# Kernel tuning notes

Hardware: AMD Instinct MI355X
Metric: run time of the kernel (lower is better)

Reference implementation:

```python
import jax, jax.numpy as jnp
import numpy as np

DIM_V = 1024
NUM_HEADS = 64            # per the module arg name; actually the per-chunk size
DIM_SPLIT = DIM_V // NUM_HEADS  # 16 = effective number of attention heads (module quirk)
N_Q, N_K = 2048, 2048
DIM_Q, DIM_K = 1024, 1024


def setup_inputs() -> dict:
    key = jax.random.key(0)
    ks = jax.random.split(key, 10)
    s = 0.02
    return {
        "Q": jax.random.normal(ks[0], (N_Q, DIM_Q), dtype=jnp.float32),
        "K": jax.random.normal(ks[1], (N_K, DIM_K), dtype=jnp.float32),
        "Wq": jax.random.normal(ks[2], (DIM_V, DIM_Q), dtype=jnp.float32) * s,
        "bq": jax.random.normal(ks[3], (DIM_V,), dtype=jnp.float32) * s,
        "Wk": jax.random.normal(ks[4], (DIM_V, DIM_K), dtype=jnp.float32) * s,
        "bk": jax.random.normal(ks[5], (DIM_V,), dtype=jnp.float32) * s,
        "Wv": jax.random.normal(ks[6], (DIM_V, DIM_K), dtype=jnp.float32) * s,
        "bv": jax.random.normal(ks[7], (DIM_V,), dtype=jnp.float32) * s,
        "Wo": jax.random.normal(ks[8], (DIM_V, DIM_V), dtype=jnp.float32) * s,
        "bo": jax.random.normal(ks[9], (DIM_V,), dtype=jnp.float32) * s,
    }


def _split_heads(x):
    # jnp.split(x[None], DIM_SPLIT, axis=2) then concat on axis 0 ==
    # [DIM_SPLIT, n, NUM_HEADS] with chunk h = x[:, h*NUM_HEADS:(h+1)*NUM_HEADS]
    n = x.shape[0]
    return x.reshape(n, DIM_SPLIT, NUM_HEADS).transpose(1, 0, 2)


def reference(Q, K, Wq, bq, Wk, bk, Wv, bv, Wo, bo):
    q = Q @ Wq.T + bq            # [n_q, dim_V]
    k = K @ Wk.T + bk            # [n_k, dim_V]
    v = K @ Wv.T + bv            # [n_k, dim_V]
    Q_ = _split_heads(q)         # [H, n_q, d] with H=DIM_SPLIT, d=NUM_HEADS
    K_ = _split_heads(k)
    V_ = _split_heads(v)
    # Faithful to source: softmax first, THEN divide by sqrt(dim_V)
    A = jax.nn.softmax(jnp.einsum('hqd,hkd->hqk', Q_, K_), axis=-1)
    A = A / jnp.sqrt(jnp.float32(DIM_V))
    O = (Q_ + jnp.einsum('hqk,hkd->hqd', A, V_)).reshape(-1, DIM_V)  # [n_q, dim_V]
    # res1 = identity (ln=False)
    O = O + jax.nn.relu(O @ Wo.T + bo)
    # res2 = identity (ln=False)
    return O
```

## Files before the change

### kernel.cpp

```cpp
#include <hip/hip_runtime.h>
#include <hip/hip_bf16.h>
#include <cstdint>

typedef unsigned short u16;
typedef __attribute__((ext_vector_type(8))) short short8;
typedef __attribute__((ext_vector_type(4))) float f32x4;

__device__ __forceinline__ u16 f2b(float f) {
  uint32_t u = __float_as_uint(f);
  u += 0x7fffu + ((u >> 16) & 1u);
  return (u16)(u >> 16);
}
__device__ __forceinline__ float b2f(u16 b) {
  return __uint_as_float(((uint32_t)b) << 16);
}
__device__ __forceinline__ uint32_t pk2bf(float a, float b) {
  __hip_bfloat162 t = __float22bfloat162_rn(make_float2(a, b));
  return *(uint32_t*)&t;
}

__global__ __launch_bounds__(256) void cast_all(
    const float* __restrict__ Q, const float* __restrict__ K,
    const float* __restrict__ Wq, const float* __restrict__ Wk,
    const float* __restrict__ Wv, const float* __restrict__ Wo,
    u16* __restrict__ xq, u16* __restrict__ xk,
    u16* __restrict__ wq, u16* __restrict__ wk,
    u16* __restrict__ wv, u16* __restrict__ wo) {
  int g = blockIdx.x * 256 + threadIdx.x;
  const float* src; u16* dst; int off;
  if      (g <  524288) { src = Q;  dst = xq; off = g; }
  else if (g < 1048576) { src = K;  dst = xk; off = g -  524288; }
  else if (g < 1310720) { src = Wq; dst = wq; off = g - 1048576; }
  else if (g < 1572864) { src = Wk; dst = wk; off = g - 1310720; }
  else if (g < 1835008) { src = Wv; dst = wv; off = g - 1572864; }
  else                  { src = Wo; dst = wo; off = g - 1835008; }
  float4 v = reinterpret_cast<const float4*>(src)[off];
  ushort4 o4;
  o4.x = f2b(v.x); o4.y = f2b(v.y); o4.z = f2b(v.z); o4.w = f2b(v.w);
  reinterpret_cast<ushort4*>(dst)[off] = o4;
}

__global__ __launch_bounds__(256) void gemm3(
    const u16* __restrict__ xq, const u16* __restrict__ xk,
    const u16* __restrict__ wq, const u16* __restrict__ wk,
    const u16* __restrict__ wv,
    const float* __restrict__ bq, const float* __restrict__ bk,
    const float* __restrict__ bv,
    u16* __restrict__ qb, u16* __restrict__ kb, u16* __restrict__ vT) {
  __shared__ __align__(16) u16 sA[128 * 40];
  __shared__ __align__(16) u16 sB[64 * 40];
  const int t = threadIdx.x, blk = blockIdx.x, z = blockIdx.y;
  const u16 *A, *B; const float* bias; u16* C; int ldC, mbase, nbase; bool brow;
  if (z == 0)      { A = xq; B = wq; bias = bq; C = qb; ldC = 1024;
                     mbase = (blk >> 4) * 128; nbase = (blk & 15) * 64; brow = false; }
  else if (z == 1) { A = xk; B = wk; bias = bk; C = kb; ldC = 1024;
                     mbase = (blk >> 4) * 128; nbase = (blk & 15) * 64; brow = false; }
  else             { A = wv; B = xk; bias = bv; C = vT; ldC = 2048;
                     mbase = (blk >> 5) * 128; nbase = (blk & 31) * 64; brow = true; }
  const int lane = t & 63, wid = t >> 6;
  const int wy = wid >> 1, wx = wid & 1;
  const int m = lane & 15, quad = lane >> 4;

  const int arow = t >> 1, acb = (t & 1) * 16;
  const int brow_ = t >> 2, bcb = (t & 3) * 8;
  const u16* gA = A + (mbase + arow) * 1024 + acb;
  const u16* gB = B + (nbase + brow_) * 1024 + bcb;

  uint4 ra0 = *(const uint4*)(gA);
  uint4 ra1 = *(const uint4*)(gA + 8);
  uint4 rb0 = *(const uint4*)(gB);

  f32x4 acc[4][2];
#pragma unroll
  for (int i = 0; i < 4; i++)
#pragma unroll
    for (int j = 0; j < 2; j++) acc[i][j] = (f32x4){0.f, 0.f, 0.f, 0.f};

  for (int kb_ = 0; kb_ < 32; ++kb_) {
    __syncthreads();
    *(uint4*)(&sA[arow * 40 + acb])     = ra0;
    *(uint4*)(&sA[arow * 40 + acb + 8]) = ra1;
    *(uint4*)(&sB[brow_ * 40 + bcb])    = rb0;
    if (kb_ < 31) {
      ra0 = *(const uint4*)(gA + (kb_ + 1) * 32);
      ra1 = *(const uint4*)(gA + (kb_ + 1) * 32 + 8);
      rb0 = *(const uint4*)(gB + (kb_ + 1) * 32);
    }
    __syncthreads();
    short8 af[4], bf[2];
#pragma unroll
    for (int mi = 0; mi < 4; mi++)
      af[mi] = *(const short8*)(&sA[(wy * 64 + mi * 16 + m) * 40 + quad * 8]);
#pragma unroll
    for (int ni = 0; ni < 2; ni++)
      bf[ni] = *(const short8*)(&sB[(wx * 32 + ni * 16 + m) * 40 + quad * 8]);
#pragma unroll
    for (int mi = 0; mi < 4; mi++)
#pragma unroll
      for (int ni = 0; ni < 2; ni++)
        acc[mi][ni] = __builtin_amdgcn_mfma_f32_16x16x32_bf16(
            af[mi], bf[ni], acc[mi][ni], 0, 0, 0);
  }

#pragma unroll
  for (int mi = 0; mi < 4; mi++)
#pragma unroll
    for (int ni = 0; ni < 2; ni++) {
      const int col = nbase + wx * 32 + ni * 16 + m;
      const float bcol = brow ? 0.f : bias[col];
#pragma unroll
      for (int r = 0; r < 4; r++) {
        const int row = mbase + wy * 64 + mi * 16 + quad * 4 + r;
        const float bval = brow ? bias[row] : bcol;
        C[row * ldC + col] = f2b(acc[mi][ni][r] + bval);
      }
    }
}

__global__ __launch_bounds__(256) void gemm_out(
    const u16* __restrict__ A, const u16* __restrict__ B,
    const float* __restrict__ bias, const u16* __restrict__ Res,
    float* __restrict__ out) {
  __shared__ __align__(16) u16 sA[64 * 40];
  __shared__ __align__(16) u16 sB[64 * 40];
  const int t = threadIdx.x, blk = blockIdx.x;
  const int mbase = (blk >> 4) * 64, nbase = (blk & 15) * 64;
  const int lane = t & 63, wid = t >> 6;
  const int wy = wid >> 1, wx = wid & 1;
  const int m = lane & 15, quad = lane >> 4;
  const int srow = t >> 2, scb = (t & 3) * 8;
  const u16* gA = A + (mbase + srow) * 1024 + scb;
  const u16* gB = B + (nbase + srow) * 1024 + scb;
  uint4 ra = *(const uint4*)gA;
  uint4 rb = *(const uint4*)gB;

  f32x4 acc[2][2];
#pragma unroll
  for (int i = 0; i < 2; i++)
#pragma unroll
    for (int j = 0; j < 2; j++) acc[i][j] = (f32x4){0.f, 0.f, 0.f, 0.f};

  for (int kb_ = 0; kb_ < 32; ++kb_) {
    __syncthreads();
    *(uint4*)(&sA[srow * 40 + scb]) = ra;
    *(uint4*)(&sB[srow * 40 + scb]) = rb;
    if (kb_ < 31) {
      ra = *(const uint4*)(gA + (kb_ + 1) * 32);
      rb = *(const uint4*)(gB + (kb_ + 1) * 32);
    }
    __syncthreads();
    short8 af[2], bf[2];
#pragma unroll
    for (int mi = 0; mi < 2; mi++)
      af[mi] = *(const short8*)(&sA[(wy * 32 + mi * 16 + m) * 40 + quad * 8]);
#pragma unroll
    for (int ni = 0; ni < 2; ni++)
      bf[ni] = *(const short8*)(&sB[(wx * 32 + ni * 16 + m) * 40 + quad * 8]);
#pragma unroll
    for (int mi = 0; mi < 2; mi++)
#pragma unroll
      for (int ni = 0; ni < 2; ni++)
        acc[mi][ni] = __builtin_amdgcn_mfma_f32_16x16x32_bf16(
            af[mi], bf[ni], acc[mi][ni], 0, 0, 0);
  }

#pragma unroll
  for (int mi = 0; mi < 2; mi++)
#pragma unroll
    for (int ni = 0; ni < 2; ni++) {
      const int col = nbase + wx * 32 + ni * 16 + m;
      const float bcol = bias[col];
#pragma unroll
      for (int r = 0; r < 4; r++) {
        const int row = mbase + wy * 32 + mi * 16 + quad * 4 + r;
        out[row * 1024 + col] =
            b2f(Res[row * 1024 + col]) + fmaxf(acc[mi][ni][r] + bcol, 0.f);
      }
    }
}

__global__ __launch_bounds__(256) void flash(
    const u16* __restrict__ q, const u16* __restrict__ k,
    const u16* __restrict__ vT, u16* __restrict__ po, float* __restrict__ lp) {
  __shared__ __align__(16) u16 sK[64 * 72];
  __shared__ __align__(16) u16 sV[64 * 72];
  __shared__ __align__(16) u16 sP[4 * 32 * 72];
  const int t = threadIdx.x;
  const int qt = blockIdx.x, h = blockIdx.y, sp = blockIdx.z;
  const int lane = t & 63, wid = t >> 6;
  const int m = lane & 15, quad = lane >> 4;
  const int colbase = h * 64;
  const int pbase = wid * 2304;
  const int kbase = sp * 512;

  short8 aq[2][2];
#pragma unroll
  for (int mi = 0; mi < 2; mi++)
#pragma unroll
    for (int g = 0; g < 2; g++)
      aq[mi][g] = *(const short8*)(
          &q[(qt * 128 + wid * 32 + mi * 16 + m) * 1024 + colbase + g * 32 + quad * 8]);

  f32x4 o[2][4];
  float lpart[2] = {0.f, 0.f};
#pragma unroll
  for (int mi = 0; mi < 2; mi++)
#pragma unroll
    for (int nt = 0; nt < 4; nt++) o[mi][nt] = (f32x4){0.f, 0.f, 0.f, 0.f};

  const int srow = t >> 2, scb = (t & 3) * 16;
  const u16* gK = k + (kbase + srow) * 1024 + colbase + scb;
  const u16* gV = vT + (colbase + srow) * 2048 + kbase + scb;

  uint4 rk0 = *(const uint4*)(gK), rk1 = *(const uint4*)(gK + 8);
  uint4 rv0 = *(const uint4*)(gV), rv1 = *(const uint4*)(gV + 8);

  uint32_t* sP32 = (uint32_t*)sP;

  for (int kt = 0; kt < 8; ++kt) {
    __syncthreads();
    *(uint4*)(&sK[srow * 72 + scb])     = rk0;
    *(uint4*)(&sK[srow * 72 + scb + 8]) = rk1;
    *(uint4*)(&sV[srow * 72 + scb])     = rv0;
    *(uint4*)(&sV[srow * 72 + scb + 8]) = rv1;
    if (kt < 7) {
      rk0 = *(const uint4*)(gK + (kt + 1) * 65536);
      rk1 = *(const uint4*)(gK + (kt + 1) * 65536 + 8);
      rv0 = *(const uint4*)(gV + (kt + 1) * 64);
      rv1 = *(const uint4*)(gV + (kt + 1) * 64 + 8);
    }
    __syncthreads();

#pragma unroll
    for (int nt = 0; nt < 4; nt++) {
      short8 bk0 = *(const short8*)(&sK[(nt * 16 + m) * 72 + quad * 8]);
      short8 bk1 = *(const short8*)(&sK[(nt * 16 + m) * 72 + 32 + quad * 8]);
#pragma unroll
      for (int mi = 0; mi < 2; mi++) {
        f32x4 st = (f32x4){0.f, 0.f, 0.f, 0.f};
        st = __builtin_amdgcn_mfma_f32_16x16x32_bf16(bk0, aq[mi][0], st, 0, 0, 0);
        st = __builtin_amdgcn_mfma_f32_16x16x32_bf16(bk1, aq[mi][1], st, 0, 0, 0);
        float p0 = __expf(st[0] - 16.0f);
        float p1 = __expf(st[1] - 16.0f);
        float p2 = __expf(st[2] - 16.0f);
        float p3 = __expf(st[3] - 16.0f);
        lpart[mi] += (p0 + p1) + (p2 + p3);
        const int pa_ = pbase + (mi * 16 + m) * 72 + nt * 16 + quad * 4;
        sP32[pa_ >> 1]       = pk2bf(p0, p1);
        sP32[(pa_ >> 1) + 1] = pk2bf(p2, p3);
      }
    }

    short8 pa[2][2];
#pragma unroll
    for (int mi = 0; mi < 2; mi++)
#pragma unroll
      for (int g = 0; g < 2; g++)
        pa[mi][g] = *(const short8*)(&sP[pbase + (mi * 16 + m) * 72 + g * 32 + quad * 8]);
#pragma unroll
    for (int nt = 0; nt < 4; nt++) {
      short8 bv0 = *(const short8*)(&sV[(nt * 16 + m) * 72 + quad * 8]);
      short8 bv1 = *(const short8*)(&sV[(nt * 16 + m) * 72 + 32 + quad * 8]);
#pragma unroll
      for (int mi = 0; mi < 2; mi++) {
        o[mi][nt] = __builtin_amdgcn_mfma_f32_16x16x32_bf16(pa[mi][0], bv0, o[mi][nt], 0, 0, 0);
        o[mi][nt] = __builtin_amdgcn_mfma_f32_16x16x32_bf16(pa[mi][1], bv1, o[mi][nt], 0, 0, 0);
      }
    }
  }

#pragma unroll
  for (int mi = 0; mi < 2; mi++) {
    float l = lpart[mi];
    l += __shfl_xor(l, 16);
    l += __shfl_xor(l, 32);
    if (quad == 0)
      lp[(sp * 16 + h) * 2048 + qt * 128 + wid * 32 + mi * 16 + m] = l;
  }

#pragma unroll
  for (int mi = 0; mi < 2; mi++)
#pragma unroll
    for (int r = 0; r < 4; r++) {
      const int qg = qt * 128 + wid * 32 + mi * 16 + quad * 4 + r;
      const int base = ((sp * 16 + h) * 2048 + qg) * 64;
#pragma unroll
      for (int nt = 0; nt < 4; nt++)
        po[base + nt * 16 + m] = f2b(o[mi][nt][r]);
    }
}

__global__ __launch_bounds__(256) void combine(
    const u16* __restrict__ po, const float* __restrict__ lp,
    const u16* __restrict__ qb, u16* __restrict__ ob) {
  const int idx = blockIdx.x * 256 + threadIdx.x;
  const int dq = idx & 15, qg = (idx >> 4) & 2047, h = idx >> 15;
  float acc0 = 0.f, acc1 = 0.f, acc2 = 0.f, acc3 = 0.f, l = 0.f;
#pragma unroll
  for (int s = 0; s < 4; s++) {
    const ushort4 p4 = *(const ushort4*)&po[(((s * 16 + h) * 2048 + qg) * 64) + dq * 4];
    acc0 += b2f(p4.x); acc1 += b2f(p4.y); acc2 += b2f(p4.z); acc3 += b2f(p4.w);
    l += lp[(s * 16 + h) * 2048 + qg];
  }
  const float inv = 1.0f / (l * 32.0f);
  const ushort4 q4 = *(const ushort4*)&qb[qg * 1024 + h * 64 + dq * 4];
  ushort4 o4;
  o4.x = f2b(b2f(q4.x) + acc0 * inv);
  o4.y = f2b(b2f(q4.y) + acc1 * inv);
  o4.z = f2b(b2f(q4.z) + acc2 * inv);
  o4.w = f2b(b2f(q4.w) + acc3 * inv);
  *(ushort4*)&ob[(h * 128 + (qg >> 4)) * 1024 + (qg & 15) * 64 + dq * 4] = o4;
}

extern "C" void kernel_launch(void* const* d_in, const int* in_sizes, int n_in,
                              void* d_out, int out_size, void* d_ws, size_t ws_size,
                              hipStream_t stream) {
  const float* Q  = (const float*)d_in[0];
  const float* K  = (const float*)d_in[1];
  const float* Wq = (const float*)d_in[2];
  const float* bq = (const float*)d_in[3];
  const float* Wk = (const float*)d_in[4];
  const float* bk = (const float*)d_in[5];
  const float* Wv = (const float*)d_in[6];
  const float* bv = (const float*)d_in[7];
  const float* Wo = (const float*)d_in[8];
  const float* bo = (const float*)d_in[9];
  float* out = (float*)d_out;

  u16* ws = (u16*)d_ws;
  u16* xq  = ws;
  u16* xk  = xq  + 2097152;
  u16* wqb = xk  + 2097152;
  u16* wkb = wqb + 1048576;
  u16* wvb = wkb + 1048576;
  u16* wob = wvb + 1048576;
  u16* qb  = wob + 1048576;
  u16* kb  = qb  + 2097152;
  u16* vT  = kb  + 2097152;
  u16* ob  = vT  + 2097152;
  u16* po  = ob  + 2097152;
  float* lp = (float*)(po + 8388608);

  cast_all<<<8192, 256, 0, stream>>>(Q, K, Wq, Wk, Wv, Wo, xq, xk, wqb, wkb, wvb, wob);

  gemm3<<<dim3(256, 3), 256, 0, stream>>>(xq, xk, wqb, wkb, wvb, bq, bk, bv, qb, kb, vT);

  flash<<<dim3(16, 16, 4), 256, 0, stream>>>(qb, kb, vT, po, lp);

  combine<<<2048, 256, 0, stream>>>(po, lp, qb, ob);

  gemm_out<<<512, 256, 0, stream>>>(ob, wob, bo, ob, out);
}
```

Measured before the change: 172.8 us.

## Keep softmax probabilities in registers and feed PV MFMA directly, dropping LDS staging

```diff
diff --git a/kernel.cpp b/kernel.cpp
--- a/kernel.cpp
+++ b/kernel.cpp
@@ -4,6 +4,7 @@
 
 typedef unsigned short u16;
 typedef __attribute__((ext_vector_type(8))) short short8;
+typedef __attribute__((ext_vector_type(4))) short short4v;
 typedef __attribute__((ext_vector_type(4))) float f32x4;
 
 __device__ __forceinline__ u16 f2b(float f) {
@@ -184,13 +185,11 @@
     const u16* __restrict__ vT, u16* __restrict__ po, float* __restrict__ lp) {
   __shared__ __align__(16) u16 sK[64 * 72];
   __shared__ __align__(16) u16 sV[64 * 72];
-  __shared__ __align__(16) u16 sP[4 * 32 * 72];
   const int t = threadIdx.x;
   const int qt = blockIdx.x, h = blockIdx.y, sp = blockIdx.z;
   const int lane = t & 63, wid = t >> 6;
   const int m = lane & 15, quad = lane >> 4;
   const int colbase = h * 64;
-  const int pbase = wid * 2304;
   const int kbase = sp * 512;
 
   short8 aq[2][2];
@@ -206,7 +205,7 @@
 #pragma unroll
   for (int mi = 0; mi < 2; mi++)
 #pragma unroll
-    for (int nt = 0; nt < 4; nt++) o[mi][nt] = (f32x4){0.f, 0.f, 0.f, 0.f};
+    for (int dt = 0; dt < 4; dt++) o[mi][dt] = (f32x4){0.f, 0.f, 0.f, 0.f};
 
   const int srow = t >> 2, scb = (t & 3) * 16;
   const u16* gK = k + (kbase + srow) * 1024 + colbase + scb;
@@ -214,8 +213,6 @@
 
   uint4 rk0 = *(const uint4*)(gK), rk1 = *(const uint4*)(gK + 8);
   uint4 rv0 = *(const uint4*)(gV), rv1 = *(const uint4*)(gV + 8);
-
-  uint32_t* sP32 = (uint32_t*)sP;
 
   for (int kt = 0; kt < 8; ++kt) {
     __syncthreads();
@@ -235,36 +232,30 @@
     for (int nt = 0; nt < 4; nt++) {
       short8 bk0 = *(const short8*)(&sK[(nt * 16 + m) * 72 + quad * 8]);
       short8 bk1 = *(const short8*)(&sK[(nt * 16 + m) * 72 + 32 + quad * 8]);
+      short4v pb[2];
 #pragma unroll
       for (int mi = 0; mi < 2; mi++) {
         f32x4 st = (f32x4){0.f, 0.f, 0.f, 0.f};
         st = __builtin_amdgcn_mfma_f32_16x16x32_bf16(bk0, aq[mi][0], st, 0, 0, 0);
         st = __builtin_amdgcn_mfma_f32_16x16x32_bf16(bk1, aq[mi][1], st, 0, 0, 0);
-        float p0 = __expf(st[0] - 16.0f);
-        float p1 = __expf(st[1] - 16.0f);
-        float p2 = __expf(st[2] - 16.0f);
-        float p3 = __expf(st[3] - 16.0f);
+        const float p0 = __expf(st[0] - 16.0f);
+        const float p1 = __expf(st[1] - 16.0f);
+        const float p2 = __expf(st[2] - 16.0f);
+        const float p3 = __expf(st[3] - 16.0f);
         lpart[mi] += (p0 + p1) + (p2 + p3);
-        const int pa_ = pbase + (mi * 16 + m) * 72 + nt * 16 + quad * 4;
-        sP32[pa_ >> 1]       = pk2bf(p0, p1);
-        sP32[(pa_ >> 1) + 1] = pk2bf(p2, p3);
+        union { uint32_t u[2]; short4v s; } pk;
+        pk.u[0] = pk2bf(p0, p1);
+        pk.u[1] = pk2bf(p2, p3);
+        pb[mi] = pk.s;
       }
-    }
-
-    short8 pa[2][2];
-#pragma unroll
-    for (int mi = 0; mi < 2; mi++)
-#pragma unroll
-      for (int g = 0; g < 2; g++)
-        pa[mi][g] = *(const short8*)(&sP[pbase + (mi * 16 + m) * 72 + g * 32 + quad * 8]);
-#pragma unroll
-    for (int nt = 0; nt < 4; nt++) {
-      short8 bv0 = *(const short8*)(&sV[(nt * 16 + m) * 72 + quad * 8]);
-      short8 bv1 = *(const short8*)(&sV[(nt * 16 + m) * 72 + 32 + quad * 8]);
-#pragma unroll
-      for (int mi = 0; mi < 2; mi++) {
-        o[mi][nt] = __builtin_amdgcn_mfma_f32_16x16x32_bf16(pa[mi][0], bv0, o[mi][nt], 0, 0, 0);
-        o[mi][nt] = __builtin_amdgcn_mfma_f32_16x16x32_bf16(pa[mi][1], bv1, o[mi][nt], 0, 0, 0);
+#pragma unroll
+      for (int dt = 0; dt < 4; dt++) {
+        const short4v va = *(const short4v*)(
+            &sV[(dt * 16 + m) * 72 + nt * 16 + quad * 4]);
+#pragma unroll
+        for (int mi = 0; mi < 2; mi++)
+          o[mi][dt] = __builtin_amdgcn_mfma_f32_16x16x16bf16_1k(
+              va, pb[mi], o[mi][dt], 0, 0, 0);
       }
     }
   }
@@ -278,16 +269,18 @@
       lp[(sp * 16 + h) * 2048 + qt * 128 + wid * 32 + mi * 16 + m] = l;
   }
 
-#pragma unroll
-  for (int mi = 0; mi < 2; mi++)
-#pragma unroll
-    for (int r = 0; r < 4; r++) {
-      const int qg = qt * 128 + wid * 32 + mi * 16 + quad * 4 + r;
-      const int base = ((sp * 16 + h) * 2048 + qg) * 64;
-#pragma unroll
-      for (int nt = 0; nt < 4; nt++)
-        po[base + nt * 16 + m] = f2b(o[mi][nt][r]);
-    }
+  uint32_t* po32 = (uint32_t*)po;
+#pragma unroll
+  for (int mi = 0; mi < 2; mi++) {
+    const int qg = qt * 128 + wid * 32 + mi * 16 + m;
+    const int base = ((sp * 16 + h) * 2048 + qg) * 64;
+#pragma unroll
+    for (int dt = 0; dt < 4; dt++) {
+      const int idx = base + dt * 16 + quad * 4;
+      po32[idx >> 1]       = pk2bf(o[mi][dt][0], o[mi][dt][1]);
+      po32[(idx >> 1) + 1] = pk2bf(o[mi][dt][2], o[mi][dt][3]);
+    }
+  }
 }
 
 __global__ __launch_bounds__(256) void combine(
```

New measurement: 179.7 us. 4.0% more time.
